# Optimization experiments

Measured on AMD Instinct MI355X. Metric: run time of the kernel, lower is better.

The kernel has to match this reference:

```python
import jax, jax.numpy as jnp
import numpy as np

T, H = 8192, 512
MC, MD = 4096, 4096
N_ENT = 128
MAX_DIST = 600  # POSITION_EMBEDDING_IN_DIM


def _make_spans(k, m, t):
    ks, kl = jax.random.split(k)
    starts = jax.random.randint(ks, (m,), 0, t - 8, dtype=jnp.int64)
    lens = jax.random.randint(kl, (m,), 0, 8, dtype=jnp.int64)
    return jnp.stack([starts, starts + lens], axis=1)  # inclusive [start, end], end < T


def setup_inputs() -> dict:
    key = jax.random.key(0)
    k = jax.random.split(key, 8)
    h = jax.random.normal(k[0], (T, H), dtype=jnp.float32)
    chem_spans = _make_spans(k[1], MC, T)
    dis_spans = _make_spans(k[2], MD, T)
    # deterministic entity assignment guarantees every entity has mentions
    chem_ent = jnp.arange(MC, dtype=jnp.int64) % N_ENT
    dis_ent = jnp.arange(MD, dtype=jnp.int64) % N_ENT
    s = 0.05
    return {
        "h": h,
        "chem_spans": chem_spans, "chem_ent": chem_ent,
        "dis_spans": dis_spans, "dis_ent": dis_ent,
        "Wc": jax.random.normal(k[3], (H, 100), jnp.float32) * s,
        "bc": jnp.zeros((100,), jnp.float32),
        "Wd": jax.random.normal(k[4], (H, 100), jnp.float32) * s,
        "bd": jnp.zeros((100,), jnp.float32),
        "Wemb": jax.random.normal(k[5], (MAX_DIST, 50), jnp.float32),
        "Ws": jax.random.normal(k[6], (250, 2), jnp.float32) * s,
        "bs": jnp.zeros((2,), jnp.float32),
        "n_chem": N_ENT,
        "n_dis": N_ENT,
    }


def reference(h, chem_spans, chem_ent, dis_spans, dis_ent,
              Wc, bc, Wd, bd, Wemb, Ws, bs, n_chem, n_dis):
    # inclusive span sums via prefix sums: sum(h[s..e]) = csum[e+1] - csum[s]
    csum = jnp.concatenate([jnp.zeros((1, h.shape[1]), h.dtype), jnp.cumsum(h, axis=0)], axis=0)
    c_sum = csum[chem_spans[:, 1] + 1] - csum[chem_spans[:, 0]]  # [MC, H]
    d_sum = csum[dis_spans[:, 1] + 1] - csum[dis_spans[:, 0]]    # [MD, H]
    c_feat = jnp.tanh(c_sum @ Wc + bc)  # [MC, 100]
    d_feat = jnp.tanh(d_sum @ Wd + bd)  # [MD, 100]
    # score Dense over concat(c, d, emb) decomposed linearly (same math)
    sc_c = c_feat @ Ws[:100]            # [MC, 2]
    sc_d = d_feat @ Ws[100:200]         # [MD, 2]
    emb_sc = Wemb @ Ws[200:250]         # [600, 2] pre-contracted embedding scores
    dist = jnp.minimum(jnp.abs(chem_spans[:, 0][:, None] - dis_spans[:, 0][None, :]),
                       MAX_DIST - 1)    # [MC, MD]
    pair = sc_c[:, None, :] + sc_d[None, :, :] + emb_sc[dist] + bs  # [MC, MD, 2]
    # running max over all mention pairs of each (chem entity, disease entity)
    pair_ids = (chem_ent[:, None] * n_dis + dis_ent[None, :]).reshape(-1)
    neg = jnp.full((n_chem * n_dis, 2), -jnp.inf, dtype=pair.dtype)
    ent_max = neg.at[pair_ids].max(pair.reshape(-1, 2))
    return jax.nn.softmax(ent_max, axis=-1).reshape(n_chem, n_dis, 2)
```

## Files before the change

### kernel.cpp

```cpp
#include <hip/hip_runtime.h>
#include <math.h>
#include <limits.h>

#define H_DIM  512
#define NFEAT  100
#define NPAD   112
#define NT     7
#define MAXD   600
#define MAXE   2048
#define CHK    64
#define DCH    64

#define NEG_ENC 0x007FFFFFu

typedef __attribute__((ext_vector_type(8))) short short8v;
typedef __attribute__((ext_vector_type(4))) float f32x4;

__device__ __forceinline__ unsigned enc_f(float f){
    unsigned u = __float_as_uint(f);
    return (u & 0x80000000u) ? ~u : (u | 0x80000000u);
}
__device__ __forceinline__ float dec_f(unsigned e){
    unsigned u = (e & 0x80000000u) ? (e ^ 0x80000000u) : ~e;
    return __uint_as_float(u);
}
__device__ __forceinline__ unsigned short f2bf(float f){
    unsigned x = __float_as_uint(f);
    return (unsigned short)((x + 0x7fffu + ((x >> 16) & 1u)) >> 16);
}

__global__ __launch_bounds__(256) void prep_kernel(
    const float* __restrict__ h,
    const float* __restrict__ Wemb, const float* __restrict__ Ws,
    const float* __restrict__ bs,
    const float* __restrict__ Wc,   const float* __restrict__ Wd,
    const int* __restrict__ cent, const int* __restrict__ dent,
    const int* __restrict__ ncp,  const int* __restrict__ ndp,
    const int* __restrict__ cspans, const int* __restrict__ dspans,
    float* __restrict__ emb2, unsigned* __restrict__ gent, int gent_n,
    unsigned short* __restrict__ Wt, unsigned short* __restrict__ hbf,
    int4* __restrict__ csorted, int4* __restrict__ dsorted,
    int MCv, int MDv, int TT, int off_e, int off_w, int off_h)
{
    const int tid = threadIdx.x;
    const int bid = blockIdx.x;

    if (bid == 0){
        __shared__ int cnt[MAXE];
        __shared__ int tmp[MAXE];
        for (int side = 0; side < 2; ++side){
            const int* ent   = side ? dent   : cent;
            const int* spans = side ? dspans : cspans;
            int4*      out   = side ? dsorted : csorted;
            const int  M     = side ? MDv : MCv;
            const int  ne    = side ? *ndp : *ncp;
            __syncthreads();
            if (ne <= MAXE){
                for (int i = tid; i < ne; i += 256) cnt[i] = 0;
                __syncthreads();
                for (int i = tid; i < M; i += 256) atomicAdd(&cnt[ent[i]], 1);
                __syncthreads();
                int* src = cnt; int* dst = tmp;
                for (int off = 1; off < ne; off <<= 1){
                    for (int i = tid; i < ne; i += 256)
                        dst[i] = src[i] + ((i >= off) ? src[i - off] : 0);
                    __syncthreads();
                    int* t_ = src; src = dst; dst = t_;
                }
                for (int i = tid; i < ne; i += 256) dst[i] = i ? src[i-1] : 0;
                __syncthreads();
                for (int i = tid; i < M; i += 256){
                    int e = ent[i];
                    int pos = atomicAdd(&dst[e], 1);
                    out[pos] = make_int4(spans[i*2], e, i, 0);
                }
            } else {
                for (int i = tid; i < M; i += 256)
                    out[i] = make_int4(spans[i*2], ent[i], i, 0);
            }
            __syncthreads();
        }
    } else if (bid < off_e){
        int i = (bid - 1) * 256 + tid;
        if (i < gent_n) gent[i] = NEG_ENC;
    } else if (bid < off_w){
        int d = (bid - off_e) * 256 + tid;
        if (d < MAXD){
            float a0 = bs[0], a1 = bs[1];
            #pragma unroll 5
            for (int q = 0; q < 50; ++q){
                float w = Wemb[d*50 + q];
                a0 += w * Ws[(200+q)*2 + 0];
                a1 += w * Ws[(200+q)*2 + 1];
            }
            emb2[d*2 + 0] = a0;
            emb2[d*2 + 1] = a1;
        }
    } else if (bid < off_h){
        const int base = (bid - off_w) * 4096;
        #pragma unroll
        for (int ii = 0; ii < 16; ++ii){
            int e = base + tid + 256*ii;
            if (e < 2*NPAD*H_DIM){
                int side = e / (NPAD*H_DIM);
                int rem  = e - side*(NPAD*H_DIM);
                int n    = rem / H_DIM;
                int k    = rem - n*H_DIM;
                const float* W = side ? Wd : Wc;
                Wt[e] = (n < NFEAT) ? f2bf(W[k*NFEAT + n]) : (unsigned short)0;
            }
        }
    } else {
        const long base = (long)(bid - off_h) * 2048 + (long)tid * 8;
        if (base < (long)TT * H_DIM){
            float4 lo = *reinterpret_cast<const float4*>(h + base);
            float4 hi = *reinterpret_cast<const float4*>(h + base + 4);
            union { unsigned short us[8]; uint4 v; } o;
            o.us[0]=f2bf(lo.x); o.us[1]=f2bf(lo.y); o.us[2]=f2bf(lo.z); o.us[3]=f2bf(lo.w);
            o.us[4]=f2bf(hi.x); o.us[5]=f2bf(hi.y); o.us[6]=f2bf(hi.z); o.us[7]=f2bf(hi.w);
            *reinterpret_cast<uint4*>(hbf + base) = o.v;
        }
    }
}

__global__ __launch_bounds__(128) void hw_gemm(
    const unsigned short* __restrict__ hbf,
    const unsigned short* __restrict__ Wt,
    float* __restrict__ HW, int mt_total, int TT)
{
    const int wid  = blockIdx.x * 2 + (threadIdx.x >> 6);
    const int lane = threadIdx.x & 63;
    const int side = wid / mt_total;
    const int mt   = wid - side * mt_total;
    if (side > 1) return;

    const unsigned short* A = hbf + (size_t)(mt*16 + (lane & 15)) * H_DIM + (lane >> 4) * 8;
    const unsigned short* B = Wt + (size_t)side * NPAD * H_DIM
                                 + (size_t)(lane & 15) * H_DIM + (lane >> 4) * 8;
    float* D = HW + (size_t)side * TT * NPAD;

    f32x4 acc[NT];
    #pragma unroll
    for (int nt = 0; nt < NT; ++nt) acc[nt] = (f32x4){0.f,0.f,0.f,0.f};

    #pragma unroll 4
    for (int ks = 0; ks < H_DIM/32; ++ks){
        short8v a = *reinterpret_cast<const short8v*>(A + ks*32);
        #pragma unroll
        for (int nt = 0; nt < NT; ++nt){
            short8v b = *reinterpret_cast<const short8v*>(B + (size_t)nt*16*H_DIM + ks*32);
            acc[nt] = __builtin_amdgcn_mfma_f32_16x16x32_bf16(a, b, acc[nt], 0, 0, 0);
        }
    }

    const int col = lane & 15;
    const int r0  = (lane >> 4) * 4;
    #pragma unroll
    for (int nt = 0; nt < NT; ++nt){
        #pragma unroll
        for (int r = 0; r < 4; ++r)
            D[(size_t)(mt*16 + r0 + r) * NPAD + nt*16 + col] = acc[nt][r];
    }
}

__global__ __launch_bounds__(128) void feat_kernel(
    const float* __restrict__ HW,
    const int* __restrict__ cspans, const int* __restrict__ dspans,
    const float* __restrict__ bc,   const float* __restrict__ bd,
    const float* __restrict__ Ws,
    float* __restrict__ sc_c, float* __restrict__ sc_d,
    int MCv, int MDv, int TT)
{
    __shared__ float red[2][2];
    const int bidx = blockIdx.x;
    const bool isd = (bidx >= MCv);
    const int  m   = isd ? (bidx - MCv) : bidx;
    const int* spans = isd ? dspans : cspans;
    const float* b   = isd ? bd : bc;
    const int  wsoff = isd ? NFEAT : 0;

    const int tid = threadIdx.x;
    const int s   = spans[m*2];
    const int len = spans[m*2 + 1] - s;

    float p0 = 0.f, p1 = 0.f;
    if (tid < NFEAT){
        const float* base = HW + (isd ? (size_t)TT*NPAD : 0) + (size_t)s*NPAD + tid;
        float v[8];
        #pragma unroll
        for (int r = 0; r < 8; ++r) v[r] = base[(size_t)r*NPAD];
        float val = 0.f;
        #pragma unroll
        for (int r = 0; r < 8; ++r) val += (r <= len) ? v[r] : 0.f;
        float f = tanhf(val + b[tid]);
        p0 = f * Ws[(wsoff + tid)*2 + 0];
        p1 = f * Ws[(wsoff + tid)*2 + 1];
    }
    #pragma unroll
    for (int k = 32; k >= 1; k >>= 1){
        p0 += __shfl_down(p0, k);
        p1 += __shfl_down(p1, k);
    }
    if ((tid & 63) == 0){ red[tid>>6][0] = p0; red[tid>>6][1] = p1; }
    __syncthreads();
    if (tid == 0){
        float* sc = isd ? sc_d : sc_c;
        sc[m*2 + 0] = red[0][0] + red[1][0];
        sc[m*2 + 1] = red[0][1] + red[1][1];
    }
}

__device__ __forceinline__ void flush_run(
    float s0, float s1, int ce, int de, int nd, bool head,
    const bool okk[6], unsigned* __restrict__ gent)
{
    float a0 = s0, a1 = s1;
    #pragma unroll
    for (int k = 0; k < 6; ++k){
        float b0 = __shfl_down(a0, 1 << k);
        float b1 = __shfl_down(a1, 1 << k);
        if (okk[k]){ a0 = fmaxf(a0, b0); a1 = fmaxf(a1, b1); }
    }
    if (head && ce != INT_MAX){
        atomicMax(&gent[(ce*nd + de)*2 + 0], enc_f(a0));
        atomicMax(&gent[(ce*nd + de)*2 + 1], enc_f(a1));
    }
}

__global__ __launch_bounds__(256) void pair_kernel(
    const int4* __restrict__ csorted, const int4* __restrict__ dsorted,
    const float* __restrict__ sc_c,   const float* __restrict__ sc_d,
    const float* __restrict__ emb2,   const int* __restrict__ ndp,
    unsigned* __restrict__ gent, int MCv, int MDv)
{
    __shared__ float2 s_e[MAXD];
    __shared__ int4   s_d[CHK];

    const int tid  = threadIdx.x;
    const int lane = tid & 63;
    const int nd   = *ndp;

    const float2* e2 = (const float2*)emb2;
    for (int i = tid; i < MAXD; i += 256) s_e[i] = e2[i];

    int   cs = 0, ce = INT_MAX;
    float c0 = 0.f, c1 = 0.f;
    {
        int ci = blockIdx.x * 256 + tid;
        if (ci < MCv){
            int4 r = csorted[ci];
            cs = r.x; ce = r.y;
            const float2 sc = *reinterpret_cast<const float2*>(&sc_c[2*r.z]);
            c0 = sc.x; c1 = sc.y;
        }
    }
    int ceprev = __shfl_up(ce, 1);
    const bool head = (lane == 0) || (ceprev != ce);
    bool okk[6];
    #pragma unroll
    for (int k = 0; k < 6; ++k) okk[k] = (__shfl_down(ce, 1 << k) == ce);

    for (int cb = blockIdx.y; cb * CHK < MDv; cb += DCH){
        const int dbase = cb * CHK;
        const int n = min(CHK, MDv - dbase);
        __syncthreads();
        for (int i = tid; i < n; i += 256){
            int4 r = dsorted[dbase + i];
            const float2 sd = *reinterpret_cast<const float2*>(&sc_d[2*r.z]);
            s_d[i] = make_int4(r.x, r.y, __float_as_int(sd.x), __float_as_int(sd.y));
        }
        __syncthreads();

        int   cur_de = s_d[0].y;
        float s0 = -INFINITY, s1 = -INFINITY;
        for (int j = 0; j < n; ++j){
            int4 dj = s_d[j];
            if (dj.y != cur_de){
                flush_run(s0, s1, ce, cur_de, nd, head, okk, gent);
                cur_de = dj.y; s0 = -INFINITY; s1 = -INFINITY;
            }
            int dd = cs - dj.x; dd = dd < 0 ? -dd : dd;
            dd = dd < (MAXD-1) ? dd : (MAXD-1);
            float2 e = s_e[dd];
            s0 = fmaxf(s0, c0 + __int_as_float(dj.z) + e.x);
            s1 = fmaxf(s1, c1 + __int_as_float(dj.w) + e.y);
        }
        flush_run(s0, s1, ce, cur_de, nd, head, okk, gent);
    }
}

__global__ void softmax_kernel(const unsigned* __restrict__ gent,
                               float* __restrict__ out, int npairs){
    int p = blockIdx.x * blockDim.x + threadIdx.x;
    if (p < npairs){
        float a = dec_f(gent[p*2 + 0]);
        float b = dec_f(gent[p*2 + 1]);
        float m = fmaxf(a, b);
        float ea = expf(a - m), eb = expf(b - m);
        float inv = 1.f / (ea + eb);
        out[p*2 + 0] = ea * inv;
        out[p*2 + 1] = eb * inv;
    }
}

extern "C" void kernel_launch(void* const* d_in, const int* in_sizes, int n_in,
                              void* d_out, int out_size, void* d_ws, size_t ws_size,
                              hipStream_t stream)
{
    const float* h      = (const float*)d_in[0];
    const int*   cspans = (const int*)  d_in[1];
    const int*   centp  = (const int*)  d_in[2];
    const int*   dspans = (const int*)  d_in[3];
    const int*   dentp  = (const int*)  d_in[4];
    const float* Wc     = (const float*)d_in[5];
    const float* bc     = (const float*)d_in[6];
    const float* Wd     = (const float*)d_in[7];
    const float* bd     = (const float*)d_in[8];
    const float* Wemb   = (const float*)d_in[9];
    const float* Ws     = (const float*)d_in[10];
    const float* bs     = (const float*)d_in[11];
    const int*   ncp    = (const int*)  d_in[12];
    const int*   ndp    = (const int*)  d_in[13];

    const int MCv    = in_sizes[1] / 2;
    const int MDv    = in_sizes[3] / 2;
    const int TT     = in_sizes[0] / H_DIM;
    const int npairs = out_size / 2;

    float*    wsf    = (float*)d_ws;
    float*    emb2   = wsf;
    float*    sc_c   = wsf + 1280;
    float*    sc_d   = sc_c + (size_t)MCv * 2;
    unsigned* gent   = (unsigned*)(sc_d + (size_t)MDv * 2);
    int4*     csorted= (int4*)(gent + out_size);
    int4*     dsorted= csorted + MCv;
    unsigned short* hbf = (unsigned short*)(dsorted + MDv);
    unsigned short* Wt  = hbf + (size_t)TT * H_DIM;
    float*    HW     = (float*)(Wt + 2 * NPAD * H_DIM);

    const int gb    = (out_size + 255) / 256;
    const int eb    = (MAXD + 255) / 256;
    const int wb    = (2*NPAD*H_DIM + 4095) / 4096;
    const int hb    = (int)(((long)TT * H_DIM + 2047) / 2048);
    const int off_e = 1 + gb;
    const int off_w = off_e + eb;
    const int off_h = off_w + wb;

    hipLaunchKernelGGL(prep_kernel, dim3(off_h + hb), dim3(256), 0, stream,
                       h, Wemb, Ws, bs, Wc, Wd, centp, dentp, ncp, ndp,
                       cspans, dspans, emb2, gent, out_size, Wt, hbf,
                       csorted, dsorted, MCv, MDv, TT, off_e, off_w, off_h);

    const int mt_total = TT / 16;
    hipLaunchKernelGGL(hw_gemm, dim3(mt_total), dim3(128), 0, stream,
                       hbf, Wt, HW, mt_total, TT);

    hipLaunchKernelGGL(feat_kernel, dim3(MCv + MDv), dim3(128), 0, stream,
                       HW, cspans, dspans, bc, bd, Ws, sc_c, sc_d, MCv, MDv, TT);

    hipLaunchKernelGGL(pair_kernel, dim3((MCv + 255)/256, DCH), dim3(256), 0, stream,
                       csorted, dsorted, sc_c, sc_d, emb2, ndp, gent, MCv, MDv);

    hipLaunchKernelGGL(softmax_kernel, dim3((npairs + 255)/256), dim3(256), 0, stream,
                       gent, (float*)d_out, npairs);
}
```

Measured before the change: 155.3 us.

## Parallelize counting sort of mentions across 32 blocks split over two kernels

Replaces the single-block counting sort in prep_kernel with a two-phase sort. Sixteen blocks per side build per-chunk histograms in prep_kernel, and 32 extra blocks appended to hw_gemm do the prefix scan and scatter, overlapping with the GEMM. This removes a serial single-block tail that likely bounded prep_kernel's duration. It costs workspace for the histograms and 16KB of static LDS in every hw_gemm block, which may reduce GEMM occupancy.

Result: faster. 134.3 us (-13.5%).

```diff
diff --git a/kernel.cpp b/kernel.cpp
--- a/kernel.cpp
+++ b/kernel.cpp
@@ -8,6 +8,7 @@
 #define NT     7
 #define MAXD   600
 #define MAXE   2048
+#define SB     16
 #define CHK    64
 #define DCH    64
 
@@ -36,52 +37,32 @@
     const float* __restrict__ Wc,   const float* __restrict__ Wd,
     const int* __restrict__ cent, const int* __restrict__ dent,
     const int* __restrict__ ncp,  const int* __restrict__ ndp,
-    const int* __restrict__ cspans, const int* __restrict__ dspans,
     float* __restrict__ emb2, unsigned* __restrict__ gent, int gent_n,
     unsigned short* __restrict__ Wt, unsigned short* __restrict__ hbf,
-    int4* __restrict__ csorted, int4* __restrict__ dsorted,
+    int* __restrict__ ghist,
     int MCv, int MDv, int TT, int off_e, int off_w, int off_h)
 {
     const int tid = threadIdx.x;
     const int bid = blockIdx.x;
 
-    if (bid == 0){
-        __shared__ int cnt[MAXE];
-        __shared__ int tmp[MAXE];
-        for (int side = 0; side < 2; ++side){
-            const int* ent   = side ? dent   : cent;
-            const int* spans = side ? dspans : cspans;
-            int4*      out   = side ? dsorted : csorted;
-            const int  M     = side ? MDv : MCv;
-            const int  ne    = side ? *ndp : *ncp;
-            __syncthreads();
-            if (ne <= MAXE){
-                for (int i = tid; i < ne; i += 256) cnt[i] = 0;
-                __syncthreads();
-                for (int i = tid; i < M; i += 256) atomicAdd(&cnt[ent[i]], 1);
-                __syncthreads();
-                int* src = cnt; int* dst = tmp;
-                for (int off = 1; off < ne; off <<= 1){
-                    for (int i = tid; i < ne; i += 256)
-                        dst[i] = src[i] + ((i >= off) ? src[i - off] : 0);
-                    __syncthreads();
-                    int* t_ = src; src = dst; dst = t_;
-                }
-                for (int i = tid; i < ne; i += 256) dst[i] = i ? src[i-1] : 0;
-                __syncthreads();
-                for (int i = tid; i < M; i += 256){
-                    int e = ent[i];
-                    int pos = atomicAdd(&dst[e], 1);
-                    out[pos] = make_int4(spans[i*2], e, i, 0);
-                }
-            } else {
-                for (int i = tid; i < M; i += 256)
-                    out[i] = make_int4(spans[i*2], ent[i], i, 0);
-            }
-            __syncthreads();
-        }
+    if (bid < 32){
+        __shared__ int hist[MAXE];
+        const int side = bid >> 4;
+        const int b    = bid & 15;
+        const int ne   = side ? *ndp : *ncp;
+        if (ne > MAXE) return;
+        const int* ent = side ? dent : cent;
+        const int  M   = side ? MDv : MCv;
+        const int chunk = (M + SB - 1) / SB;
+        const int i0 = b * chunk, i1 = min(M, i0 + chunk);
+        for (int e = tid; e < ne; e += 256) hist[e] = 0;
+        __syncthreads();
+        for (int i = i0 + tid; i < i1; i += 256) atomicAdd(&hist[ent[i]], 1);
+        __syncthreads();
+        int* gh = ghist + (side*SB + b) * MAXE;
+        for (int e = tid; e < ne; e += 256) gh[e] = hist[e];
     } else if (bid < off_e){
-        int i = (bid - 1) * 256 + tid;
+        int i = (bid - 32) * 256 + tid;
         if (i < gent_n) gent[i] = NEG_ENC;
     } else if (bid < off_w){
         int d = (bid - off_e) * 256 + tid;
@@ -126,8 +107,79 @@
 __global__ __launch_bounds__(128) void hw_gemm(
     const unsigned short* __restrict__ hbf,
     const unsigned short* __restrict__ Wt,
-    float* __restrict__ HW, int mt_total, int TT)
-{
+    float* __restrict__ HW, int mt_total, int TT,
+    const int* __restrict__ cent, const int* __restrict__ dent,
+    const int* __restrict__ ncp,  const int* __restrict__ ndp,
+    const int* __restrict__ cspans, const int* __restrict__ dspans,
+    const int* __restrict__ ghist,
+    int4* __restrict__ csorted, int4* __restrict__ dsorted,
+    int MCv, int MDv)
+{
+    __shared__ int s_tot[MAXE];
+    __shared__ int s_cur[MAXE];
+    __shared__ int s_wsum[2];
+
+    if ((int)blockIdx.x >= mt_total){
+        const int sb   = blockIdx.x - mt_total;
+        const int side = sb >> 4;
+        const int b    = sb & 15;
+        const int tid  = threadIdx.x;
+        const int ne   = side ? *ndp : *ncp;
+        const int* ent = side ? dent : cent;
+        const int* spans = side ? dspans : cspans;
+        int4* out      = side ? dsorted : csorted;
+        const int M    = side ? MDv : MCv;
+        const int chunk = (M + SB - 1) / SB;
+        const int i0 = b * chunk, i1 = min(M, i0 + chunk);
+
+        if (ne <= MAXE){
+            const int* gh = ghist + side*SB*MAXE;
+            for (int e = tid; e < ne; e += 128){
+                int pre = 0, tot = 0;
+                #pragma unroll
+                for (int bb = 0; bb < SB; ++bb){
+                    int v = gh[bb*MAXE + e];
+                    tot += v;
+                    pre += (bb < b) ? v : 0;
+                }
+                s_tot[e] = tot;
+                s_cur[e] = pre;
+            }
+            __syncthreads();
+            const int per = (ne + 127) / 128;
+            const int lo = min(tid*per, ne), hi = min(lo + per, ne);
+            int sum = 0;
+            for (int j = lo; j < hi; ++j) sum += s_tot[j];
+            const int lane = tid & 63, w = tid >> 6;
+            int x = sum;
+            #pragma unroll
+            for (int k = 1; k < 64; k <<= 1){
+                int y = __shfl_up(x, k);
+                if (lane >= k) x += y;
+            }
+            int excl = x - sum;
+            if (lane == 63) s_wsum[w] = x;
+            __syncthreads();
+            if (w == 1) excl += s_wsum[0];
+            int run = excl;
+            for (int j = lo; j < hi; ++j){
+                int t = s_tot[j];
+                s_cur[j] += run;
+                run += t;
+            }
+            __syncthreads();
+            for (int i = i0 + tid; i < i1; i += 128){
+                int e = ent[i];
+                int pos = atomicAdd(&s_cur[e], 1);
+                out[pos] = make_int4(spans[i*2], e, i, 0);
+            }
+        } else {
+            for (int i = i0 + tid; i < i1; i += 128)
+                out[i] = make_int4(spans[i*2], ent[i], i, 0);
+        }
+        return;
+    }
+
     const int wid  = blockIdx.x * 2 + (threadIdx.x >> 6);
     const int lane = threadIdx.x & 63;
     const int side = wid / mt_total;
@@ -336,24 +388,27 @@
     int4*     dsorted= csorted + MCv;
     unsigned short* hbf = (unsigned short*)(dsorted + MDv);
     unsigned short* Wt  = hbf + (size_t)TT * H_DIM;
-    float*    HW     = (float*)(Wt + 2 * NPAD * H_DIM);
+    int*      ghist  = (int*)(Wt + 2 * NPAD * H_DIM);
+    float*    HW     = (float*)(ghist + 2 * SB * MAXE);
 
     const int gb    = (out_size + 255) / 256;
     const int eb    = (MAXD + 255) / 256;
     const int wb    = (2*NPAD*H_DIM + 4095) / 4096;
     const int hb    = (int)(((long)TT * H_DIM + 2047) / 2048);
-    const int off_e = 1 + gb;
+    const int off_e = 32 + gb;
     const int off_w = off_e + eb;
     const int off_h = off_w + wb;
 
     hipLaunchKernelGGL(prep_kernel, dim3(off_h + hb), dim3(256), 0, stream,
                        h, Wemb, Ws, bs, Wc, Wd, centp, dentp, ncp, ndp,
-                       cspans, dspans, emb2, gent, out_size, Wt, hbf,
-                       csorted, dsorted, MCv, MDv, TT, off_e, off_w, off_h);
+                       emb2, gent, out_size, Wt, hbf, ghist,
+                       MCv, MDv, TT, off_e, off_w, off_h);
 
     const int mt_total = TT / 16;
-    hipLaunchKernelGGL(hw_gemm, dim3(mt_total), dim3(128), 0, stream,
-                       hbf, Wt, HW, mt_total, TT);
+    hipLaunchKernelGGL(hw_gemm, dim3(mt_total + 32), dim3(128), 0, stream,
+                       hbf, Wt, HW, mt_total, TT,
+                       centp, dentp, ncp, ndp, cspans, dspans,
+                       ghist, csorted, dsorted, MCv, MDv);
 
     hipLaunchKernelGGL(feat_kernel, dim3(MCv + MDv), dim3(128), 0, stream,
                        HW, cspans, dspans, bc, bd, Ws, sc_c, sc_d, MCv, MDv, TT);
```
